# Kernel optimization log

Hardware: AMD Instinct MI355X
Metric: run time of the kernel (lower is better)

The kernel has to match this reference:

```python
import jax, jax.numpy as jnp
import numpy as np

NUM_HEADS = 8


def setup_inputs() -> dict:
    key = jax.random.key(0)
    k1, k2, k3, k4, k5 = jax.random.split(key, 5)
    N, L, D = 256, 512, 256
    x = jax.random.normal(k1, (N, L, D), dtype=jnp.float32)
    dist_bias = jax.random.normal(k2, (N, N), dtype=jnp.float32)
    w_qkv = jax.random.normal(k3, (3 * D, D), dtype=jnp.float32) * (D ** -0.5)
    w_proj = jax.random.normal(k4, (D, D), dtype=jnp.float32) * (D ** -0.5)
    b_proj = jax.random.normal(k5, (D,), dtype=jnp.float32) * 0.02
    return {"x": x, "dist_bias": dist_bias, "w_qkv": w_qkv,
            "w_proj": w_proj, "b_proj": b_proj}


def reference(x, dist_bias, w_qkv, w_proj, b_proj):
    # x: (N, L, D)  attention over the SAMPLE axis N, per (head, position)
    N, L, D = x.shape
    H = NUM_HEADS
    hd = D // H
    scale = hd ** -0.5

    qkv = jnp.einsum('nld,ed->nle', x, w_qkv)              # (N, L, 3D)
    qkv = qkv.reshape(N, L, 3, H, hd)
    q = jnp.transpose(qkv[:, :, 0], (2, 1, 0, 3))          # (H, L, N, hd)
    k = jnp.transpose(qkv[:, :, 1], (2, 1, 0, 3))
    v = jnp.transpose(qkv[:, :, 2], (2, 1, 0, 3))

    # scores over sample axis, with additive genetic-distance bias
    scores = jnp.einsum('hlnd,hlmd->hlnm', q, k) * scale   # (H, L, N, N)
    scores = scores + dist_bias[None, None, :, :]
    attn = jax.nn.softmax(scores, axis=-1)                 # dropout p=0.0

    out = jnp.einsum('hlnm,hlmd->hlnd', attn, v)           # (H, L, N, hd)
    out = jnp.transpose(out, (2, 1, 0, 3)).reshape(N, L, D)
    return jnp.einsum('nld,ed->nle', out, w_proj) + b_proj
```

## Files before the change

### kernel.cpp

```cpp
#include <hip/hip_runtime.h>
#include <stdint.h>

#define NS 256
#define LS 512
#define DS 256
#define HS 8
#define HD 32
#define SCALE 0.17677669529663687f
#define LOG2E 1.4426950408889634f
#define QSCALE (SCALE * LOG2E)

typedef __attribute__((ext_vector_type(4))) float f32x4;
typedef __attribute__((ext_vector_type(8))) __bf16 bf16x8;
typedef __attribute__((ext_vector_type(8))) unsigned short ushort8;

static __device__ __forceinline__ unsigned short f2bf(float f) {
  unsigned int u = __builtin_bit_cast(unsigned int, f);
  u += 0x7fffu + ((u >> 16) & 1u);
  return (unsigned short)(u >> 16);
}

static __device__ __forceinline__ void gld16(const void* g, void* l) {
  __builtin_amdgcn_global_load_lds((const __attribute__((address_space(1))) void*)g,
                                   (__attribute__((address_space(3))) void*)l, 16, 0, 0);
}

static __device__ __forceinline__ f32x4 mfma16(bf16x8 a, bf16x8 b, f32x4 c) {
  return __builtin_amdgcn_mfma_f32_16x16x32_bf16(a, b, c, 0, 0, 0);
}

__global__ void k_cvt(const float* __restrict__ in, unsigned short* __restrict__ out, int n) {
  int stride = gridDim.x * blockDim.x;
  for (int i = blockIdx.x * blockDim.x + threadIdx.x; i * 8 < n; i += stride) {
    int b = i * 8;
    float4 a0 = *(const float4*)(in + b);
    float4 a1 = *(const float4*)(in + b + 4);
    ushort8 o;
    o[0] = f2bf(a0.x); o[1] = f2bf(a0.y); o[2] = f2bf(a0.z); o[3] = f2bf(a0.w);
    o[4] = f2bf(a1.x); o[5] = f2bf(a1.y); o[6] = f2bf(a1.z); o[7] = f2bf(a1.w);
    *(ushort8*)(out + b) = o;
  }
}

__global__ void k_bt(const float* __restrict__ d, float* __restrict__ bT) {
  int i = blockIdx.x * 256 + threadIdx.x;
  int r = i >> 8, c = i & 255;
  bT[(size_t)c * NS + r] = d[i] * LOG2E;
}

__global__ __launch_bounds__(256) void k_qkv(const unsigned short* __restrict__ xb,
                                             const unsigned short* __restrict__ wq,
                                             unsigned short* __restrict__ qkv) {
  __shared__ unsigned short As[128 * 64];
  __shared__ unsigned short Bs[128 * 64];
  const int tid = threadIdx.x, lane = tid & 63, wid = tid >> 6;
  const int bid = blockIdx.x;
  const int et = bid % 6, rt = bid / 6;
  const int l = rt >> 1, n0 = (rt & 1) << 7;
  const int wr = wid >> 1, wc = wid & 1;

  f32x4 acc[4][4] = {};
  const int rowA = lane >> 3;
  const int kkA = (lane & 7) * 8;

  for (int kt = 0; kt < 4; ++kt) {
    __syncthreads();
    const int k0 = kt * 64;
    for (int p = 0; p < 4; ++p) {
      const int chunk = p * 4 + wid;
      const int row = chunk * 8 + rowA;
      const unsigned short* gA = xb + (((size_t)(n0 + row)) * LS + l) * DS + k0 + kkA;
      gld16(gA, &As[chunk * 8 * 64]);
      const unsigned short* gB = wq + ((size_t)(et * 128 + row)) * DS + k0 + kkA;
      gld16(gB, &Bs[chunk * 8 * 64]);
    }
    __syncthreads();
    for (int kf = 0; kf < 2; ++kf) {
      const int ko = kf * 32 + (lane >> 4) * 8;
      bf16x8 a[4], b[4];
      for (int m = 0; m < 4; ++m)
        a[m] = *(const bf16x8*)&As[(wr * 64 + m * 16 + (lane & 15)) * 64 + ko];
      for (int nn = 0; nn < 4; ++nn)
        b[nn] = *(const bf16x8*)&Bs[(wc * 64 + nn * 16 + (lane & 15)) * 64 + ko];
      for (int m = 0; m < 4; ++m)
        for (int nn = 0; nn < 4; ++nn)
          acc[m][nn] = mfma16(a[m], b[nn], acc[m][nn]);
    }
  }

  const int rbase = (lane >> 4) * 4, cbase = lane & 15;
  for (int m = 0; m < 4; ++m)
    for (int nn = 0; nn < 4; ++nn) {
      const int e = et * 128 + wc * 64 + nn * 16 + cbase;
      const int which = e >> 8, h = (e >> 5) & 7, d = e & 31;
      const float qs = (which == 0) ? QSCALE : 1.0f;
      const size_t base = (((size_t)which * HS + h) * LS + l) * (NS * HD) + d;
      for (int j = 0; j < 4; ++j) {
        const int n = n0 + wr * 64 + m * 16 + rbase + j;
        qkv[base + (size_t)n * HD] = f2bf(acc[m][nn][j] * qs);
      }
    }
}

__global__ __launch_bounds__(256) void k_attn(const unsigned short* __restrict__ qkv,
                                              const float* __restrict__ bT,
                                              unsigned short* __restrict__ att) {
  __shared__ unsigned short Vt[32][NS + 8];
  __shared__ unsigned short Pl[4][16][72];
  const int tid = threadIdx.x, lane = tid & 63, wid = tid >> 6;
  const int h = blockIdx.x >> 9, l = blockIdx.x & 511;
  const unsigned short* qb = qkv + (((size_t)0 * HS + h) * LS + l) * (NS * HD);
  const unsigned short* kb = qkv + (((size_t)1 * HS + h) * LS + l) * (NS * HD);
  const unsigned short* vb = qkv + (((size_t)2 * HS + h) * LS + l) * (NS * HD);

  {
    const unsigned short* vr = vb + tid * HD;
    for (int c = 0; c < 4; ++c) {
      ushort8 v8 = *(const ushort8*)(vr + c * 8);
      for (int jj = 0; jj < 8; ++jj) Vt[c * 8 + jj][tid] = v8[jj];
    }
  }

  const int wbase = wid * 64, fr = lane & 15, g = lane >> 4, fk = g * 8;
  bf16x8 qf[4];
#pragma unroll
  for (int m = 0; m < 4; ++m)
    qf[m] = *(const bf16x8*)(qb + (size_t)(wbase + m * 16 + fr) * HD + fk);

  f32x4 o[4][2] = {};
  float mo[4][4], ls[4][4];
#pragma unroll
  for (int m = 0; m < 4; ++m)
#pragma unroll
    for (int j = 0; j < 4; ++j) { mo[m][j] = -1e30f; ls[m][j] = 0.f; }

  __syncthreads();

  for (int cb = 0; cb < 4; ++cb) {
    const int c0 = cb * 64;
    bf16x8 kfr[4];
#pragma unroll
    for (int nn = 0; nn < 4; ++nn)
      kfr[nn] = *(const bf16x8*)(kb + (size_t)(c0 + nn * 16 + fr) * HD + fk);

#pragma unroll
    for (int m = 0; m < 4; ++m) {
      float4 bfv[4];
#pragma unroll
      for (int nn = 0; nn < 4; ++nn)
        bfv[nn] = *(const float4*)(bT + (size_t)(c0 + nn * 16 + fr) * NS + wbase + m * 16 + g * 4);

      f32x4 z = {};
      f32x4 s[4];
#pragma unroll
      for (int nn = 0; nn < 4; ++nn) s[nn] = mfma16(qf[m], kfr[nn], z);

#pragma unroll
      for (int j = 0; j < 4; ++j) {
        float mx = fmaxf(fmaxf(s[0][j], s[1][j]), fmaxf(s[2][j], s[3][j]));
#pragma unroll
        for (int off = 1; off < 16; off <<= 1) mx = fmaxf(mx, __shfl_xor(mx, off));
        const float mn = fmaxf(mo[m][j], mx);
        const float f = __builtin_exp2f(mo[m][j] - mn);
        mo[m][j] = mn;
        float rs = 0.f;
#pragma unroll
        for (int nn = 0; nn < 4; ++nn) {
          const float bj = (j == 0) ? bfv[nn].x : (j == 1) ? bfv[nn].y
                         : (j == 2) ? bfv[nn].z : bfv[nn].w;
          float p = __builtin_exp2f(s[nn][j] - mn + bj);
          rs += p;
          Pl[wid][g * 4 + j][nn * 16 + fr] = f2bf(p);
        }
#pragma unroll
        for (int off = 1; off < 16; off <<= 1) rs += __shfl_xor(rs, off);
        ls[m][j] = ls[m][j] * f + rs;
        o[m][0][j] *= f;
        o[m][1][j] *= f;
      }

#pragma unroll
      for (int kf = 0; kf < 2; ++kf) {
        const int ko = kf * 32 + fk;
        bf16x8 pa = *(const bf16x8*)&Pl[wid][fr][ko];
#pragma unroll
        for (int df = 0; df < 2; ++df) {
          bf16x8 vv = *(const bf16x8*)&Vt[df * 16 + fr][c0 + ko];
          o[m][df] = mfma16(pa, vv, o[m][df]);
        }
      }
    }
  }

#pragma unroll
  for (int m = 0; m < 4; ++m)
#pragma unroll
    for (int j = 0; j < 4; ++j) {
      const float inv = 1.0f / ls[m][j];
      const int n = wbase + m * 16 + g * 4 + j;
      const size_t ob = ((size_t)n * LS + l) * DS + h * HD;
      att[ob + 0 * 16 + fr] = f2bf(o[m][0][j] * inv);
      att[ob + 1 * 16 + fr] = f2bf(o[m][1][j] * inv);
    }
}

__global__ __launch_bounds__(256) void k_proj(const unsigned short* __restrict__ ab,
                                              const unsigned short* __restrict__ wp,
                                              const float* __restrict__ bp,
                                              float* __restrict__ out) {
  __shared__ unsigned short As[128 * 64];
  __shared__ unsigned short Bs[128 * 64];
  const int tid = threadIdx.x, lane = tid & 63, wid = tid >> 6;
  const int bid = blockIdx.x;
  const int et = bid & 1, rt = bid >> 1;
  const int wr = wid >> 1, wc = wid & 1;

  f32x4 acc[4][4] = {};
  const int rowA = lane >> 3;
  const int kkA = (lane & 7) * 8;

  for (int kt = 0; kt < 4; ++kt) {
    __syncthreads();
    const int k0 = kt * 64;
    for (int p = 0; p < 4; ++p) {
      const int chunk = p * 4 + wid;
      const int row = chunk * 8 + rowA;
      const unsigned short* gA = ab + ((size_t)(rt * 128 + row)) * DS + k0 + kkA;
      gld16(gA, &As[chunk * 8 * 64]);
      const unsigned short* gB = wp + ((size_t)(et * 128 + row)) * DS + k0 + kkA;
      gld16(gB, &Bs[chunk * 8 * 64]);
    }
    __syncthreads();
    for (int kf = 0; kf < 2; ++kf) {
      const int ko = kf * 32 + (lane >> 4) * 8;
      bf16x8 a[4], b[4];
      for (int m = 0; m < 4; ++m)
        a[m] = *(const bf16x8*)&As[(wr * 64 + m * 16 + (lane & 15)) * 64 + ko];
      for (int nn = 0; nn < 4; ++nn)
        b[nn] = *(const bf16x8*)&Bs[(wc * 64 + nn * 16 + (lane & 15)) * 64 + ko];
      for (int m = 0; m < 4; ++m)
        for (int nn = 0; nn < 4; ++nn)
          acc[m][nn] = mfma16(a[m], b[nn], acc[m][nn]);
    }
  }

  const int rbase = (lane >> 4) * 4, cbase = lane & 15;
  for (int m = 0; m < 4; ++m)
    for (int nn = 0; nn < 4; ++nn) {
      const int e = et * 128 + wc * 64 + nn * 16 + cbase;
      const float bv = bp[e];
      for (int j = 0; j < 4; ++j) {
        const size_t mm = (size_t)rt * 128 + wr * 64 + m * 16 + rbase + j;
        out[mm * DS + e] = acc[m][nn][j] + bv;
      }
    }
}

extern "C" void kernel_launch(void* const* d_in, const int* in_sizes, int n_in,
                              void* d_out, int out_size, void* d_ws, size_t ws_size,
                              hipStream_t stream) {
  const float* x     = (const float*)d_in[0];
  const float* dist  = (const float*)d_in[1];
  const float* wqkv  = (const float*)d_in[2];
  const float* wproj = (const float*)d_in[3];
  const float* bproj = (const float*)d_in[4];
  float* out = (float*)d_out;

  unsigned short* ws   = (unsigned short*)d_ws;
  unsigned short* xb   = ws;
  unsigned short* wqb  = xb + 33554432;
  unsigned short* wpb  = wqb + 196608;
  unsigned short* qkvb = wpb + 65536;
  unsigned short* attb = qkvb + 100663296;
  float* bTf           = (float*)(attb + 33554432);

  k_cvt<<<8192, 256, 0, stream>>>(x, xb, 33554432);
  k_cvt<<<96, 256, 0, stream>>>(wqkv, wqb, 196608);
  k_cvt<<<32, 256, 0, stream>>>(wproj, wpb, 65536);
  k_bt<<<256, 256, 0, stream>>>(dist, bTf);
  k_qkv<<<6144, 256, 0, stream>>>(xb, wqb, qkvb);
  k_attn<<<4096, 256, 0, stream>>>(qkvb, bTf, attb);
  k_proj<<<2048, 256, 0, stream>>>(attb, wpb, bproj, out);
}
```

Baseline: 665.6 us.

## Transpose score MFMA to row-major softmax, split attention blocks, drop bias transpose

The attention kernel now computes scores as K·Q so each lane holds a query row across four key columns. This makes the row max and sum need only two cross-lane shuffles, and lets P be packed and stored as bf16x4 vectors. The dist bias is read directly in row-major layout and scaled by LOG2E with an FMA, which removes the separate transpose kernel. Each (h,l) is split into two blocks of 128 queries with launch bounds targeting 4 blocks per SIMD. In exchange, V is transposed into LDS twice per (h,l), and the row rescale factors need extra shuffles.

```diff
diff --git a/kernel.cpp b/kernel.cpp
--- a/kernel.cpp
+++ b/kernel.cpp
@@ -12,6 +12,7 @@
 
 typedef __attribute__((ext_vector_type(4))) float f32x4;
 typedef __attribute__((ext_vector_type(8))) __bf16 bf16x8;
+typedef __attribute__((ext_vector_type(4))) __bf16 bf16x4;
 typedef __attribute__((ext_vector_type(8))) unsigned short ushort8;
 
 static __device__ __forceinline__ unsigned short f2bf(float f) {
@@ -42,12 +43,6 @@
   }
 }
 
-__global__ void k_bt(const float* __restrict__ d, float* __restrict__ bT) {
-  int i = blockIdx.x * 256 + threadIdx.x;
-  int r = i >> 8, c = i & 255;
-  bT[(size_t)c * NS + r] = d[i] * LOG2E;
-}
-
 __global__ __launch_bounds__(256) void k_qkv(const unsigned short* __restrict__ xb,
                                              const unsigned short* __restrict__ wq,
                                              unsigned short* __restrict__ qkv) {
@@ -102,13 +97,15 @@
     }
 }
 
-__global__ __launch_bounds__(256) void k_attn(const unsigned short* __restrict__ qkv,
-                                              const float* __restrict__ bT,
-                                              unsigned short* __restrict__ att) {
+__global__ __launch_bounds__(256, 4) void k_attn(const unsigned short* __restrict__ qkv,
+                                                 const float* __restrict__ dist,
+                                                 unsigned short* __restrict__ att) {
   __shared__ unsigned short Vt[32][NS + 8];
-  __shared__ unsigned short Pl[4][16][72];
+  __shared__ __bf16 Pl[4][16][68];
   const int tid = threadIdx.x, lane = tid & 63, wid = tid >> 6;
-  const int h = blockIdx.x >> 9, l = blockIdx.x & 511;
+  const int bid = blockIdx.x;
+  const int h = bid >> 10, l = (bid >> 1) & 511, half = bid & 1;
+  const int n0 = half << 7;
   const unsigned short* qb = qkv + (((size_t)0 * HS + h) * LS + l) * (NS * HD);
   const unsigned short* kb = qkv + (((size_t)1 * HS + h) * LS + l) * (NS * HD);
   const unsigned short* vb = qkv + (((size_t)2 * HS + h) * LS + l) * (NS * HD);
@@ -121,18 +118,15 @@
     }
   }
 
-  const int wbase = wid * 64, fr = lane & 15, g = lane >> 4, fk = g * 8;
-  bf16x8 qf[4];
-#pragma unroll
-  for (int m = 0; m < 4; ++m)
-    qf[m] = *(const bf16x8*)(qb + (size_t)(wbase + m * 16 + fr) * HD + fk);
-
-  f32x4 o[4][2] = {};
-  float mo[4][4], ls[4][4];
-#pragma unroll
-  for (int m = 0; m < 4; ++m)
-#pragma unroll
-    for (int j = 0; j < 4; ++j) { mo[m][j] = -1e30f; ls[m][j] = 0.f; }
+  const int fr = lane & 15, g = lane >> 4, fk = g * 8;
+  const int wq0 = n0 + wid * 32;
+  bf16x8 qf[2];
+#pragma unroll
+  for (int m = 0; m < 2; ++m)
+    qf[m] = *(const bf16x8*)(qb + (size_t)(wq0 + m * 16 + fr) * HD + fk);
+
+  f32x4 o[2][2] = {};
+  float mo[2] = {-1e30f, -1e30f}, ls[2] = {0.f, 0.f};
 
   __syncthreads();
 
@@ -144,39 +138,57 @@
       kfr[nn] = *(const bf16x8*)(kb + (size_t)(c0 + nn * 16 + fr) * HD + fk);
 
 #pragma unroll
-    for (int m = 0; m < 4; ++m) {
-      float4 bfv[4];
+    for (int m = 0; m < 2; ++m) {
+      const int qg = wq0 + m * 16 + fr;
+      float4 bv[4];
 #pragma unroll
       for (int nn = 0; nn < 4; ++nn)
-        bfv[nn] = *(const float4*)(bT + (size_t)(c0 + nn * 16 + fr) * NS + wbase + m * 16 + g * 4);
+        bv[nn] = *(const float4*)(dist + (size_t)qg * NS + c0 + nn * 16 + g * 4);
 
       f32x4 z = {};
       f32x4 s[4];
 #pragma unroll
-      for (int nn = 0; nn < 4; ++nn) s[nn] = mfma16(qf[m], kfr[nn], z);
+      for (int nn = 0; nn < 4; ++nn) s[nn] = mfma16(kfr[nn], qf[m], z);
+
+      float mx = -1e30f;
+#pragma unroll
+      for (int nn = 0; nn < 4; ++nn) {
+#pragma unroll
+        for (int j = 0; j < 4; ++j) {
+          const float b = (j == 0) ? bv[nn].x : (j == 1) ? bv[nn].y
+                        : (j == 2) ? bv[nn].z : bv[nn].w;
+          const float v = fmaf(b, LOG2E, s[nn][j]);
+          s[nn][j] = v;
+          mx = fmaxf(mx, v);
+        }
+      }
+      mx = fmaxf(mx, __shfl_xor(mx, 16));
+      mx = fmaxf(mx, __shfl_xor(mx, 32));
+      const float mn = fmaxf(mo[m], mx);
+      const float fsc = __builtin_exp2f(mo[m] - mn);
+      mo[m] = mn;
+
+      float rs = 0.f;
+#pragma unroll
+      for (int nn = 0; nn < 4; ++nn) {
+        bf16x4 pk;
+#pragma unroll
+        for (int j = 0; j < 4; ++j) {
+          const float p = __builtin_exp2f(s[nn][j] - mn);
+          rs += p;
+          pk[j] = (__bf16)p;
+        }
+        *(bf16x4*)&Pl[wid][fr][nn * 16 + g * 4] = pk;
+      }
+      rs += __shfl_xor(rs, 16);
+      rs += __shfl_xor(rs, 32);
+      ls[m] = ls[m] * fsc + rs;
 
 #pragma unroll
       for (int j = 0; j < 4; ++j) {
-        float mx = fmaxf(fmaxf(s[0][j], s[1][j]), fmaxf(s[2][j], s[3][j]));
-#pragma unroll
-        for (int off = 1; off < 16; off <<= 1) mx = fmaxf(mx, __shfl_xor(mx, off));
-        const float mn = fmaxf(mo[m][j], mx);
-        const float f = __builtin_exp2f(mo[m][j] - mn);
-        mo[m][j] = mn;
-        float rs = 0.f;
-#pragma unroll
-        for (int nn = 0; nn < 4; ++nn) {
-          const float bj = (j == 0) ? bfv[nn].x : (j == 1) ? bfv[nn].y
-                         : (j == 2) ? bfv[nn].z : bfv[nn].w;
-          float p = __builtin_exp2f(s[nn][j] - mn + bj);
-          rs += p;
-          Pl[wid][g * 4 + j][nn * 16 + fr] = f2bf(p);
-        }
-#pragma unroll
-        for (int off = 1; off < 16; off <<= 1) rs += __shfl_xor(rs, off);
-        ls[m][j] = ls[m][j] * f + rs;
-        o[m][0][j] *= f;
-        o[m][1][j] *= f;
+        const float fo = __shfl(fsc, g * 4 + j);
+        o[m][0][j] *= fo;
+        o[m][1][j] *= fo;
       }
 
 #pragma unroll
@@ -193,15 +205,17 @@
   }
 
 #pragma unroll
-  for (int m = 0; m < 4; ++m)
+  for (int m = 0; m < 2; ++m) {
+    const float inv = 1.0f / ls[m];
 #pragma unroll
     for (int j = 0; j < 4; ++j) {
-      const float inv = 1.0f / ls[m][j];
-      const int n = wbase + m * 16 + g * 4 + j;
+      const float invo = __shfl(inv, g * 4 + j);
+      const int n = wq0 + m * 16 + g * 4 + j;
       const size_t ob = ((size_t)n * LS + l) * DS + h * HD;
-      att[ob + 0 * 16 + fr] = f2bf(o[m][0][j] * inv);
-      att[ob + 1 * 16 + fr] = f2bf(o[m][1][j] * inv);
-    }
+      att[ob + 0 * 16 + fr] = f2bf(o[m][0][j] * invo);
+      att[ob + 1 * 16 + fr] = f2bf(o[m][1][j] * invo);
+    }
+  }
 }
 
 __global__ __launch_bounds__(256) void k_proj(const unsigned short* __restrict__ ab,
@@ -272,13 +286,11 @@
   unsigned short* wpb  = wqb + 196608;
   unsigned short* qkvb = wpb + 65536;
   unsigned short* attb = qkvb + 100663296;
-  float* bTf           = (float*)(attb + 33554432);
 
   k_cvt<<<8192, 256, 0, stream>>>(x, xb, 33554432);
   k_cvt<<<96, 256, 0, stream>>>(wqkv, wqb, 196608);
   k_cvt<<<32, 256, 0, stream>>>(wproj, wpb, 65536);
-  k_bt<<<256, 256, 0, stream>>>(dist, bTf);
   k_qkv<<<6144, 256, 0, stream>>>(xb, wqb, qkvb);
-  k_attn<<<4096, 256, 0, stream>>>(qkvb, bTf, attb);
+  k_attn<<<8192, 256, 0, stream>>>(qkvb, dist, attb);
   k_proj<<<2048, 256, 0, stream>>>(attb, wpb, bproj, out);
 }
```

Measured after the change: 562.6 us. 15.5% less time.
